# Optimization experiments

Hardware: AMD Instinct MI355X
Metric: run time of the kernel (lower is better)

Reference implementation:

```python
import jax, jax.numpy as jnp
import numpy as np

B, N, P, F = 4, 131072, 512, 32  # batch, points per batch, plane_size, feature_dim


def setup_inputs() -> dict:
    key = jax.random.key(0)
    k1, k2 = jax.random.split(key)
    coords = jax.random.uniform(k1, (B, N, 3), jnp.float32, -1.0, 1.0)
    # torch.nn.init.uniform_(tplanes, -0.01, 0.01)
    tplanes = jax.random.uniform(k2, (3, P, P, F), jnp.float32, -0.01, 0.01)
    return {"coords": coords, "tplanes": tplanes}


def _bilerp(plane, uv):
    # plane: [P, P, F] laid out [H(v), W(u), C]; uv: [M, 2] in [0, 1]
    # matches nvdiffrast texture(filter_mode='linear', boundary_mode='clamp',
    # max_mip_level=0): texel centers at (i + 0.5) / P, clamp-to-edge.
    Ps = plane.shape[0]
    x = jnp.clip(uv[:, 0] * Ps - 0.5, 0.0, Ps - 1.0)
    y = jnp.clip(uv[:, 1] * Ps - 0.5, 0.0, Ps - 1.0)
    x0f = jnp.floor(x)
    y0f = jnp.floor(y)
    xi0 = x0f.astype(jnp.int32)
    yi0 = y0f.astype(jnp.int32)
    xi1 = jnp.minimum(xi0 + 1, Ps - 1)
    yi1 = jnp.minimum(yi0 + 1, Ps - 1)
    fx = (x - x0f)[:, None]  # [M, 1]
    fy = (y - y0f)[:, None]
    f00 = plane[yi0, xi0]  # [M, F]
    f01 = plane[yi0, xi1]
    f10 = plane[yi1, xi0]
    f11 = plane[yi1, xi1]
    return (f00 * (1.0 - fx) + f01 * fx) * (1.0 - fy) + (f10 * (1.0 - fx) + f11 * fx) * fy


def reference(coords, tplanes):
    batch_size = coords.shape[0]
    c = coords * 0.5 + 0.5          # [-1,1] -> [0,1]
    c = c.reshape(-1, 3)            # [M, 3]
    # plane 0 samples (x, y); plane 1 samples (x, z); plane 2 samples (z, y)
    uvs = jnp.stack([c[:, (0, 1)], c[:, (0, 2)], c[:, (2, 1)]], axis=0)  # [3, M, 2]
    feats = jax.vmap(_bilerp)(tplanes, uvs)        # [3, M, F]
    feats = jnp.transpose(feats, (1, 0, 2))        # [M, 3, F]
    out = feats.reshape(batch_size, -1, 3 * F)     # concat over planes: [B, N, 3F]
    return out
```

## Files before the change

kernel.cpp:

```cpp
#include <hip/hip_runtime.h>


#define PS 512
#define FDIM 32

__global__ __launch_bounds__(256) void tplanes_enc_kernel(
    const float* __restrict__ coords,
    const float* __restrict__ tplanes,
    float* __restrict__ out,
    int M)
{
    int tid = blockIdx.x * blockDim.x + threadIdx.x;
    int total = M * 3 * (FDIM / 4);
    if (tid >= total) return;

    int chunk = tid & 7;
    int pp    = tid >> 3;
    int plane = pp % 3;
    int point = pp / 3;

    float cx = coords[point * 3 + 0] * 0.5f + 0.5f;
    float cy = coords[point * 3 + 1] * 0.5f + 0.5f;
    float cz = coords[point * 3 + 2] * 0.5f + 0.5f;

    float u = (plane == 2) ? cz : cx;
    float v = (plane == 1) ? cz : cy;

    float x = fminf(fmaxf(u * (float)PS - 0.5f, 0.0f), (float)(PS - 1));
    float y = fminf(fmaxf(v * (float)PS - 0.5f, 0.0f), (float)(PS - 1));
    float x0f = floorf(x);
    float y0f = floorf(y);
    int xi0 = (int)x0f;
    int yi0 = (int)y0f;
    int xi1 = min(xi0 + 1, PS - 1);
    int yi1 = min(yi0 + 1, PS - 1);
    float fx = x - x0f;
    float fy = y - y0f;

    const float4* base = (const float4*)(tplanes + (size_t)plane * PS * PS * FDIM);
    int o00 = (yi0 * PS + xi0) * 8 + chunk;
    int o01 = (yi0 * PS + xi1) * 8 + chunk;
    int o10 = (yi1 * PS + xi0) * 8 + chunk;
    int o11 = (yi1 * PS + xi1) * 8 + chunk;

    float4 f00 = base[o00];
    float4 f01 = base[o01];
    float4 f10 = base[o10];
    float4 f11 = base[o11];

    float gx = 1.0f - fx;
    float gy = 1.0f - fy;
    float4 r;
    r.x = (f00.x * gx + f01.x * fx) * gy + (f10.x * gx + f11.x * fx) * fy;
    r.y = (f00.y * gx + f01.y * fx) * gy + (f10.y * gx + f11.y * fx) * fy;
    r.z = (f00.z * gx + f01.z * fx) * gy + (f10.z * gx + f11.z * fx) * fy;
    r.w = (f00.w * gx + f01.w * fx) * gy + (f10.w * gx + f11.w * fx) * fy;

    ((float4*)out)[(size_t)pp * 8 + chunk] = r;
}

extern "C" void kernel_launch(void* const* d_in, const int* in_sizes, int n_in,
                              void* d_out, int out_size, void* d_ws, size_t ws_size,
                              hipStream_t stream) {
    const float* coords  = (const float*)d_in[0];
    const float* tplanes = (const float*)d_in[1];
    float* out = (float*)d_out;

    int M = in_sizes[0] / 3;
    int total = M * 3 * (FDIM / 4);
    int block = 256;
    int grid = (total + block - 1) / block;
    tplanes_enc_kernel<<<grid, block, 0, stream>>>(coords, tplanes, out, M);
}
```

Baseline: 355.2 us.

## Sort points by Morton cell before gathering triplane features

Adds a counting sort over a 16^3 Morton grid (histogram, scan, scatter) so the main gather kernel handles spatially coherent points, which should improve cache locality on the random texel fetches. The main kernel also interleaves block order across the grid and writes output with nontemporal stores into the original point positions. The cost is four extra launches plus a memset, atomics, and scattered output writes. It falls back to the direct kernel when the workspace is too small.

```diff
diff --git a/kernel.cpp b/kernel.cpp
--- a/kernel.cpp
+++ b/kernel.cpp
@@ -3,28 +3,99 @@
 
 #define PS 512
 #define FDIM 32
+#define GRID1D 16
+#define NCELLS (GRID1D * GRID1D * GRID1D)
 
-__global__ __launch_bounds__(256) void tplanes_enc_kernel(
-    const float* __restrict__ coords,
-    const float* __restrict__ tplanes,
-    float* __restrict__ out,
-    int M)
-{
-    int tid = blockIdx.x * blockDim.x + threadIdx.x;
-    int total = M * 3 * (FDIM / 4);
-    if (tid >= total) return;
+typedef float f32x4 __attribute__((ext_vector_type(4)));
+
+__device__ __forceinline__ int cell_of(float c01) {
+    int i = (int)(c01 * (float)GRID1D);
+    return min(max(i, 0), GRID1D - 1);
+}
+
+__device__ __forceinline__ unsigned part3_4(unsigned x) {
+    x = (x | (x << 4)) & 0xC3u;
+    x = (x | (x << 2)) & 0x249u;
+    return x;
+}
+
+__device__ __forceinline__ unsigned morton12(int ix, int iy, int iz) {
+    return part3_4((unsigned)ix) | (part3_4((unsigned)iy) << 1) | (part3_4((unsigned)iz) << 2);
+}
+
+__device__ __forceinline__ unsigned key_of_point(const float* __restrict__ coords, int p,
+                                                 float& cx, float& cy, float& cz) {
+    cx = coords[p * 3 + 0] * 0.5f + 0.5f;
+    cy = coords[p * 3 + 1] * 0.5f + 0.5f;
+    cz = coords[p * 3 + 2] * 0.5f + 0.5f;
+    return morton12(cell_of(cx), cell_of(cy), cell_of(cz));
+}
+
+__global__ __launch_bounds__(256) void k_hist(const float* __restrict__ coords,
+                                              unsigned* __restrict__ hist, int M) {
+    int p = blockIdx.x * blockDim.x + threadIdx.x;
+    if (p >= M) return;
+    float cx, cy, cz;
+    unsigned key = key_of_point(coords, p, cx, cy, cz);
+    atomicAdd(&hist[key], 1u);
+}
+
+__global__ __launch_bounds__(1024) void k_scan(unsigned* __restrict__ hist) {
+    __shared__ unsigned part[1024];
+    int t = threadIdx.x;
+    unsigned v0 = hist[t * 4 + 0];
+    unsigned v1 = hist[t * 4 + 1];
+    unsigned v2 = hist[t * 4 + 2];
+    unsigned v3 = hist[t * 4 + 3];
+    unsigned local = v0 + v1 + v2 + v3;
+    part[t] = local;
+    __syncthreads();
+    for (int off = 1; off < 1024; off <<= 1) {
+        unsigned x = (t >= off) ? part[t - off] : 0u;
+        __syncthreads();
+        part[t] += x;
+        __syncthreads();
+    }
+    unsigned excl = part[t] - local;
+    hist[t * 4 + 0] = excl;
+    hist[t * 4 + 1] = excl + v0;
+    hist[t * 4 + 2] = excl + v0 + v1;
+    hist[t * 4 + 3] = excl + v0 + v1 + v2;
+}
+
+__global__ __launch_bounds__(256) void k_scatter(const float* __restrict__ coords,
+                                                 unsigned* __restrict__ offs,
+                                                 float4* __restrict__ scoords, int M) {
+    int p = blockIdx.x * blockDim.x + threadIdx.x;
+    if (p >= M) return;
+    float cx, cy, cz;
+    unsigned key = key_of_point(coords, p, cx, cy, cz);
+    unsigned slot = atomicAdd(&offs[key], 1u);
+    float4 v;
+    v.x = cx; v.y = cy; v.z = cz; v.w = __int_as_float(p);
+    scoords[slot] = v;
+}
+
+__global__ __launch_bounds__(256) void k_main(const float4* __restrict__ scoords,
+                                              const float* __restrict__ tplanes,
+                                              float* __restrict__ out, int M) {
+    int nb = gridDim.x;
+    int chunkB = nb >> 3;
+    int b = blockIdx.x;
+    int b2 = (b & 7) * chunkB + (b >> 3);
+    int tid = b2 * 256 + (int)threadIdx.x;
 
     int chunk = tid & 7;
-    int pp    = tid >> 3;
+    int pp = tid >> 3;
     int plane = pp % 3;
-    int point = pp / 3;
+    int spos = pp / 3;
+    if (spos >= M) return;
 
-    float cx = coords[point * 3 + 0] * 0.5f + 0.5f;
-    float cy = coords[point * 3 + 1] * 0.5f + 0.5f;
-    float cz = coords[point * 3 + 2] * 0.5f + 0.5f;
+    float4 c4 = scoords[spos];
+    int p = __float_as_int(c4.w);
 
-    float u = (plane == 2) ? cz : cx;
-    float v = (plane == 1) ? cz : cy;
+    float u = (plane == 2) ? c4.z : c4.x;
+    float v = (plane == 1) ? c4.z : c4.y;
 
     float x = fminf(fmaxf(u * (float)PS - 0.5f, 0.0f), (float)(PS - 1));
     float y = fminf(fmaxf(v * (float)PS - 0.5f, 0.0f), (float)(PS - 1));
@@ -50,12 +121,49 @@
 
     float gx = 1.0f - fx;
     float gy = 1.0f - fy;
+    f32x4 r;
+    r.x = (f00.x * gx + f01.x * fx) * gy + (f10.x * gx + f11.x * fx) * fy;
+    r.y = (f00.y * gx + f01.y * fx) * gy + (f10.y * gx + f11.y * fx) * fy;
+    r.z = (f00.z * gx + f01.z * fx) * gy + (f10.z * gx + f11.z * fx) * fy;
+    r.w = (f00.w * gx + f01.w * fx) * gy + (f10.w * gx + f11.w * fx) * fy;
+
+    f32x4* outv = (f32x4*)out;
+    __builtin_nontemporal_store(r, &outv[(size_t)p * 24 + plane * 8 + chunk]);
+}
+
+__global__ __launch_bounds__(256) void k_direct(const float* __restrict__ coords,
+                                                const float* __restrict__ tplanes,
+                                                float* __restrict__ out, int M) {
+    int tid = blockIdx.x * blockDim.x + threadIdx.x;
+    int total = M * 3 * (FDIM / 4);
+    if (tid >= total) return;
+    int chunk = tid & 7;
+    int pp = tid >> 3;
+    int plane = pp % 3;
+    int point = pp / 3;
+    float cx = coords[point * 3 + 0] * 0.5f + 0.5f;
+    float cy = coords[point * 3 + 1] * 0.5f + 0.5f;
+    float cz = coords[point * 3 + 2] * 0.5f + 0.5f;
+    float u = (plane == 2) ? cz : cx;
+    float v = (plane == 1) ? cz : cy;
+    float x = fminf(fmaxf(u * (float)PS - 0.5f, 0.0f), (float)(PS - 1));
+    float y = fminf(fmaxf(v * (float)PS - 0.5f, 0.0f), (float)(PS - 1));
+    float x0f = floorf(x);
+    float y0f = floorf(y);
+    int xi0 = (int)x0f, yi0 = (int)y0f;
+    int xi1 = min(xi0 + 1, PS - 1), yi1 = min(yi0 + 1, PS - 1);
+    float fx = x - x0f, fy = y - y0f;
+    const float4* base = (const float4*)(tplanes + (size_t)plane * PS * PS * FDIM);
+    float4 f00 = base[(yi0 * PS + xi0) * 8 + chunk];
+    float4 f01 = base[(yi0 * PS + xi1) * 8 + chunk];
+    float4 f10 = base[(yi1 * PS + xi0) * 8 + chunk];
+    float4 f11 = base[(yi1 * PS + xi1) * 8 + chunk];
+    float gx = 1.0f - fx, gy = 1.0f - fy;
     float4 r;
     r.x = (f00.x * gx + f01.x * fx) * gy + (f10.x * gx + f11.x * fx) * fy;
     r.y = (f00.y * gx + f01.y * fx) * gy + (f10.y * gx + f11.y * fx) * fy;
     r.z = (f00.z * gx + f01.z * fx) * gy + (f10.z * gx + f11.z * fx) * fy;
     r.w = (f00.w * gx + f01.w * fx) * gy + (f10.w * gx + f11.w * fx) * fy;
-
     ((float4*)out)[(size_t)pp * 8 + chunk] = r;
 }
 
@@ -67,8 +175,25 @@
     float* out = (float*)d_out;
 
     int M = in_sizes[0] / 3;
+    size_t need = (size_t)NCELLS * 4 + (size_t)M * 16;
+
+    if (ws_size < need) {
+        int total = M * 3 * (FDIM / 4);
+        k_direct<<<(total + 255) / 256, 256, 0, stream>>>(coords, tplanes, out, M);
+        return;
+    }
+
+    unsigned* hist = (unsigned*)d_ws;
+    float4* scoords = (float4*)((char*)d_ws + NCELLS * 4);
+
+    (void)hipMemsetAsync(hist, 0, NCELLS * 4, stream);
+
+    int pb = (M + 255) / 256;
+    k_hist<<<pb, 256, 0, stream>>>(coords, hist, M);
+    k_scan<<<1, 1024, 0, stream>>>(hist);
+    k_scatter<<<pb, 256, 0, stream>>>(coords, hist, scoords, M);
+
     int total = M * 3 * (FDIM / 4);
-    int block = 256;
-    int grid = (total + block - 1) / block;
-    tplanes_enc_kernel<<<grid, block, 0, stream>>>(coords, tplanes, out, M);
+    int nb = total / 256;
+    k_main<<<nb, 256, 0, stream>>>(scoords, tplanes, out, M);
 }
```

New measurement: 410.7 us. 1.16x slower.
